# Kernel optimization log

Measured on AMD Instinct MI355X. Metric: run time of the kernel, lower is better.

## Reference

```python
import jax, jax.numpy as jnp
import numpy as np

B, S, D, H = 4, 2048, 1024, 16


def setup_inputs() -> dict:
    key = jax.random.key(0)
    ks = jax.random.split(key, 9)
    scale = 0.02  # keep logits in a sane range
    x = jax.random.normal(ks[0], (B, S, D), dtype=jnp.float32)
    Wq = jax.random.normal(ks[1], (D, D), dtype=jnp.float32) * scale
    bq = jax.random.normal(ks[2], (D,), dtype=jnp.float32) * scale
    Wk = jax.random.normal(ks[3], (D, D), dtype=jnp.float32) * scale
    bk = jax.random.normal(ks[4], (D,), dtype=jnp.float32) * scale
    Wv = jax.random.normal(ks[5], (D, D), dtype=jnp.float32) * scale
    bv = jax.random.normal(ks[6], (D,), dtype=jnp.float32) * scale
    Wo = jax.random.normal(ks[7], (D, D), dtype=jnp.float32) * scale
    bo = jax.random.normal(ks[8], (D,), dtype=jnp.float32) * scale
    return {"x": x, "Wq": Wq, "bq": bq, "Wk": Wk, "bk": bk,
            "Wv": Wv, "bv": bv, "Wo": Wo, "bo": bo}


def _apply_rope(x):
    """Rotate-half RoPE over the full feature dim (applied pre-projection)."""
    b, s, d = x.shape
    half = d // 2
    # theta_i = 10000^(-2i/d), i in [0, d/2)
    freq = jnp.exp(jnp.arange(0, d, 2, dtype=jnp.float32) * (-np.log(10000.0) / d))
    ang = jnp.arange(s, dtype=jnp.float32)[:, None] * freq[None, :]  # [S, d/2]
    cos, sin = jnp.cos(ang), jnp.sin(ang)
    x1, x2 = x[..., :half], x[..., half:]
    return jnp.concatenate([x1 * cos - x2 * sin, x1 * sin + x2 * cos], axis=-1)


def reference(x, Wq, bq, Wk, bk, Wv, bv, Wo, bo):
    b, s, d = x.shape
    h = H
    hd = d // h
    rx = _apply_rope(x)  # [B, S, D]

    def proj(W, bias):
        y = rx @ W.T + bias                       # torch Linear: x W^T + b
        return y.reshape(b, s, h, hd).transpose(0, 2, 1, 3)  # [B, H, S, hd]

    q, k, v = proj(Wq, bq), proj(Wk, bk), proj(Wv, bv)
    scores = jnp.einsum('bhqd,bhkd->bhqk', q, k) / np.sqrt(hd)
    attn = jax.nn.softmax(scores, axis=-1)
    attended = jnp.einsum('bhqk,bhkd->bhqd', attn, v)
    attended = attended.transpose(0, 2, 1, 3).reshape(b, s, d)
    return attended @ Wo.T + bo
```

## Files before the change

### kernel.cpp

```cpp
#include <hip/hip_runtime.h>

#define NB 4
#define NS 2048
#define ND 1024
#define NH 16
#define HD 64

using bf16x8 = __attribute__((ext_vector_type(8))) short;
using f32x4  = __attribute__((ext_vector_type(4))) float;

__device__ __forceinline__ unsigned short f2bf(float f) {
  union { float f; unsigned u; } a; a.f = f;
  unsigned r = a.u + 0x7FFF + ((a.u >> 16) & 1);
  return (unsigned short)(r >> 16);
}

__device__ __forceinline__ void gload_lds16(const void* g, void* l) {
  __builtin_amdgcn_global_load_lds(
      (const __attribute__((address_space(1))) void*)g,
      (__attribute__((address_space(3))) void*)l, 16, 0, 0);
}

__global__ __launch_bounds__(256) void rope_kernel(const float* __restrict__ x,
                                                   unsigned short* __restrict__ rx) {
  int idx = blockIdx.x * 256 + threadIdx.x;
  int j  = idx & 511;
  int bs = idx >> 9;
  int s  = bs & (NS - 1);
  const float* xp = x + (size_t)bs * ND;
  float ang = (float)s * __expf((float)j * -0.017988946039f);
  float sn, cs;
  __sincosf(ang, &sn, &cs);
  float x1 = xp[j], x2 = xp[j + 512];
  unsigned short* rp = rx + (size_t)bs * ND;
  rp[j]       = f2bf(x1 * cs - x2 * sn);
  rp[j + 512] = f2bf(x1 * sn + x2 * cs);
}

__global__ __launch_bounds__(256) void wconv_kernel(const float* __restrict__ w0,
                                                    const float* __restrict__ w1,
                                                    const float* __restrict__ w2,
                                                    const float* __restrict__ w3,
                                                    unsigned short* __restrict__ wb) {
  int idx = blockIdx.x * 256 + threadIdx.x;
  int e = idx << 2;
  const float* w = (e < (1 << 20)) ? w0 : (e < (2 << 20)) ? w1 : (e < (3 << 20)) ? w2 : w3;
  float4 v = *(const float4*)(w + (e & 0xFFFFF));
  ushort4 o;
  o.x = f2bf(v.x); o.y = f2bf(v.y); o.z = f2bf(v.z); o.w = f2bf(v.w);
  *(ushort4*)(wb + e) = o;
}

__global__ __launch_bounds__(256) void gemm_qkv(const unsigned short* __restrict__ A,
                                                const unsigned short* __restrict__ Wb,
                                                const float* __restrict__ bq,
                                                const float* __restrict__ bk,
                                                const float* __restrict__ bv,
                                                unsigned short* __restrict__ q,
                                                unsigned short* __restrict__ k,
                                                unsigned short* __restrict__ vt) {
  __shared__ alignas(16) unsigned short As[128 * 32];
  __shared__ alignas(16) unsigned short Bs[128 * 32];
  const int tid = threadIdx.x;
  const int lane = tid & 63;
  const int wid = tid >> 6;
  const int wm = wid >> 1, wn = wid & 1;
  const int l15 = lane & 15, lg = lane >> 4;
  const int m0 = blockIdx.x * 128;
  const int n0 = blockIdx.y * 128;
  const int z = blockIdx.z;
  const unsigned short* Bp = Wb + ((size_t)z << 20);

  f32x4 acc[4][4] = {};

  for (int k0 = 0; k0 < ND; k0 += 32) {
#pragma unroll
    for (int it = 0; it < 2; ++it) {
      int c = it * 256 + tid;
      int row = c >> 2, kc = (c & 3) << 3;
      int ldsbase = (it * 256 + (tid & 192)) << 3;
      gload_lds16(A  + (size_t)(m0 + row) * ND + k0 + kc, As + ldsbase);
      gload_lds16(Bp + (size_t)(n0 + row) * ND + k0 + kc, Bs + ldsbase);
    }
    __syncthreads();
    bf16x8 af[4], bfr[4];
#pragma unroll
    for (int m = 0; m < 4; ++m)
      af[m] = *(const bf16x8*)(As + (wm * 64 + m * 16 + l15) * 32 + lg * 8);
#pragma unroll
    for (int n = 0; n < 4; ++n)
      bfr[n] = *(const bf16x8*)(Bs + (wn * 64 + n * 16 + l15) * 32 + lg * 8);
#pragma unroll
    for (int m = 0; m < 4; ++m)
#pragma unroll
      for (int n = 0; n < 4; ++n)
        acc[m][n] = __builtin_amdgcn_mfma_f32_16x16x32_bf16(af[m], bfr[n], acc[m][n], 0, 0, 0);
    __syncthreads();
  }

  const float* bias = (z == 0) ? bq : (z == 1) ? bk : bv;
#pragma unroll
  for (int n = 0; n < 4; ++n) {
    int col = n0 + wn * 64 + n * 16 + l15;
    float bb = bias[col];
    int hh = col >> 6, dd = col & 63;
#pragma unroll
    for (int m = 0; m < 4; ++m) {
#pragma unroll
      for (int r = 0; r < 4; ++r) {
        int rowi = m0 + wm * 64 + m * 16 + lg * 4 + r;
        int bbi = rowi >> 11, ss = rowi & (NS - 1);
        unsigned short val = f2bf(acc[m][n][r] + bb);
        size_t bhoff = (size_t)(bbi * NH + hh);
        if (z == 0)      q [(bhoff * NS + ss) * HD + dd] = val;
        else if (z == 1) k [(bhoff * NS + ss) * HD + dd] = val;
        else             vt[(bhoff * HD + dd) * NS + ss] = val;
      }
    }
  }
}

__global__ __launch_bounds__(256) void attn_kernel(const unsigned short* __restrict__ q,
                                                   const unsigned short* __restrict__ k,
                                                   const unsigned short* __restrict__ vt,
                                                   unsigned short* __restrict__ att) {
  __shared__ alignas(16) unsigned short Ks[64 * 64];
  __shared__ alignas(16) unsigned short Vs[64 * 64];
  __shared__ alignas(16) unsigned short Ps[4][32 * 64];
  const int tid = threadIdx.x;
  const int lane = tid & 63;
  const int w = tid >> 6;
  const int l15 = lane & 15, lg = lane >> 4;
  const int bh = blockIdx.y;
  const int b = bh >> 4, h = bh & 15;
  const int q0 = blockIdx.x * 128;
  const unsigned short* qp = q  + (size_t)bh * NS * HD;
  const unsigned short* kp = k  + (size_t)bh * NS * HD;
  const unsigned short* vp = vt + (size_t)bh * HD * NS;

  bf16x8 qf[2][2];
#pragma unroll
  for (int m = 0; m < 2; ++m)
#pragma unroll
    for (int t = 0; t < 2; ++t)
      qf[m][t] = *(const bf16x8*)(qp + (size_t)(q0 + w * 32 + m * 16 + l15) * HD + t * 32 + lg * 8);

  f32x4 o[2][4] = {};
  float run_m[2][4], run_l[2][4];
#pragma unroll
  for (int m = 0; m < 2; ++m)
#pragma unroll
    for (int r = 0; r < 4; ++r) { run_m[m][r] = -1e30f; run_l[m][r] = 0.f; }

  unsigned short* ps = &Ps[w][0];

  for (int t0 = 0; t0 < NS; t0 += 64) {
#pragma unroll
    for (int it = 0; it < 2; ++it) {
      int c = it * 256 + tid;
      int ro = c >> 3, cc = (c & 7) << 3;
      int ldsbase = (it * 256 + (tid & 192)) << 3;
      gload_lds16(kp + (size_t)(t0 + ro) * HD + cc, Ks + ldsbase);
      gload_lds16(vp + (size_t)ro * NS + t0 + cc,   Vs + ldsbase);
    }
    __syncthreads();

    f32x4 sc[2][4] = {};
#pragma unroll
    for (int kk = 0; kk < 2; ++kk)
#pragma unroll
      for (int n = 0; n < 4; ++n) {
        bf16x8 kf = *(const bf16x8*)(Ks + (n * 16 + l15) * HD + kk * 32 + lg * 8);
#pragma unroll
        for (int m = 0; m < 2; ++m)
          sc[m][n] = __builtin_amdgcn_mfma_f32_16x16x32_bf16(qf[m][kk], kf, sc[m][n], 0, 0, 0);
      }

#pragma unroll
    for (int m = 0; m < 2; ++m)
#pragma unroll
      for (int r = 0; r < 4; ++r) {
        float mx = fmaxf(fmaxf(sc[m][0][r], sc[m][1][r]), fmaxf(sc[m][2][r], sc[m][3][r]));
        mx = fmaxf(mx, __shfl_xor(mx, 1));
        mx = fmaxf(mx, __shfl_xor(mx, 2));
        mx = fmaxf(mx, __shfl_xor(mx, 4));
        mx = fmaxf(mx, __shfl_xor(mx, 8));
        float nm = fmaxf(run_m[m][r], mx);
        float fac = __expf(0.125f * (run_m[m][r] - nm));
        run_m[m][r] = nm;
        float rs = 0.f;
#pragma unroll
        for (int n = 0; n < 4; ++n) {
          float p = __expf(0.125f * (sc[m][n][r] - nm));
          sc[m][n][r] = p;
          rs += p;
        }
        rs += __shfl_xor(rs, 1);
        rs += __shfl_xor(rs, 2);
        rs += __shfl_xor(rs, 4);
        rs += __shfl_xor(rs, 8);
        run_l[m][r] = run_l[m][r] * fac + rs;
#pragma unroll
        for (int n = 0; n < 4; ++n) o[m][n][r] *= fac;
      }

#pragma unroll
    for (int m = 0; m < 2; ++m)
#pragma unroll
      for (int n = 0; n < 4; ++n)
#pragma unroll
        for (int r = 0; r < 4; ++r)
          ps[(m * 16 + lg * 4 + r) * 64 + n * 16 + l15] = f2bf(sc[m][n][r]);

    bf16x8 pf[2][2];
#pragma unroll
    for (int m = 0; m < 2; ++m)
#pragma unroll
      for (int kk = 0; kk < 2; ++kk)
        pf[m][kk] = *(const bf16x8*)(ps + (m * 16 + l15) * 64 + kk * 32 + lg * 8);

#pragma unroll
    for (int kk = 0; kk < 2; ++kk)
#pragma unroll
      for (int n = 0; n < 4; ++n) {
        bf16x8 vf = *(const bf16x8*)(Vs + (n * 16 + l15) * HD + kk * 32 + lg * 8);
#pragma unroll
        for (int m = 0; m < 2; ++m)
          o[m][n] = __builtin_amdgcn_mfma_f32_16x16x32_bf16(pf[m][kk], vf, o[m][n], 0, 0, 0);
      }
    __syncthreads();
  }

#pragma unroll
  for (int m = 0; m < 2; ++m)
#pragma unroll
    for (int r = 0; r < 4; ++r) {
      int rowi = q0 + w * 32 + m * 16 + lg * 4 + r;
      float inv = 1.0f / run_l[m][r];
#pragma unroll
      for (int n = 0; n < 4; ++n)
        att[((size_t)(b * NS + rowi)) * ND + h * HD + n * 16 + l15] = f2bf(o[m][n][r] * inv);
    }
}

__global__ __launch_bounds__(256) void gemm_out(const unsigned short* __restrict__ A,
                                                const unsigned short* __restrict__ Bw,
                                                const float* __restrict__ bo,
                                                float* __restrict__ out) {
  __shared__ alignas(16) unsigned short As[128 * 32];
  __shared__ alignas(16) unsigned short Bs[128 * 32];
  const int tid = threadIdx.x;
  const int lane = tid & 63;
  const int wid = tid >> 6;
  const int wm = wid >> 1, wn = wid & 1;
  const int l15 = lane & 15, lg = lane >> 4;
  const int m0 = blockIdx.x * 128;
  const int n0 = blockIdx.y * 128;

  f32x4 acc[4][4] = {};

  for (int k0 = 0; k0 < ND; k0 += 32) {
#pragma unroll
    for (int it = 0; it < 2; ++it) {
      int c = it * 256 + tid;
      int row = c >> 2, kc = (c & 3) << 3;
      int ldsbase = (it * 256 + (tid & 192)) << 3;
      gload_lds16(A  + (size_t)(m0 + row) * ND + k0 + kc, As + ldsbase);
      gload_lds16(Bw + (size_t)(n0 + row) * ND + k0 + kc, Bs + ldsbase);
    }
    __syncthreads();
    bf16x8 af[4], bfr[4];
#pragma unroll
    for (int m = 0; m < 4; ++m)
      af[m] = *(const bf16x8*)(As + (wm * 64 + m * 16 + l15) * 32 + lg * 8);
#pragma unroll
    for (int n = 0; n < 4; ++n)
      bfr[n] = *(const bf16x8*)(Bs + (wn * 64 + n * 16 + l15) * 32 + lg * 8);
#pragma unroll
    for (int m = 0; m < 4; ++m)
#pragma unroll
      for (int n = 0; n < 4; ++n)
        acc[m][n] = __builtin_amdgcn_mfma_f32_16x16x32_bf16(af[m], bfr[n], acc[m][n], 0, 0, 0);
    __syncthreads();
  }

#pragma unroll
  for (int n = 0; n < 4; ++n) {
    int col = n0 + wn * 64 + n * 16 + l15;
    float bb = bo[col];
#pragma unroll
    for (int m = 0; m < 4; ++m)
#pragma unroll
      for (int r = 0; r < 4; ++r) {
        int rowi = m0 + wm * 64 + m * 16 + lg * 4 + r;
        out[(size_t)rowi * ND + col] = acc[m][n][r] + bb;
      }
  }
}

extern "C" void kernel_launch(void* const* d_in, const int* in_sizes, int n_in,
                              void* d_out, int out_size, void* d_ws, size_t ws_size,
                              hipStream_t stream) {
  const float* x  = (const float*)d_in[0];
  const float* Wq = (const float*)d_in[1];
  const float* bq = (const float*)d_in[2];
  const float* Wk = (const float*)d_in[3];
  const float* bk = (const float*)d_in[4];
  const float* Wv = (const float*)d_in[5];
  const float* bv = (const float*)d_in[6];
  const float* Wo = (const float*)d_in[7];
  const float* bo = (const float*)d_in[8];
  float* out = (float*)d_out;

  char* ws = (char*)d_ws;
  const size_t MB = 1024 * 1024;
  unsigned short* rx  = (unsigned short*)(ws);
  unsigned short* wb  = (unsigned short*)(ws + 16 * MB);
  unsigned short* qb  = (unsigned short*)(ws + 24 * MB);
  unsigned short* kb  = (unsigned short*)(ws + 40 * MB);
  unsigned short* vtb = (unsigned short*)(ws + 56 * MB);
  unsigned short* att = (unsigned short*)(ws + 72 * MB);

  rope_kernel<<<dim3(16384), dim3(256), 0, stream>>>(x, rx);
  wconv_kernel<<<dim3(4096), dim3(256), 0, stream>>>(Wq, Wk, Wv, Wo, wb);
  gemm_qkv<<<dim3(64, 8, 3), dim3(256), 0, stream>>>(rx, wb, bq, bk, bv, qb, kb, vtb);
  attn_kernel<<<dim3(16, 64), dim3(256), 0, stream>>>(qb, kb, vtb, att);
  gemm_out<<<dim3(64, 8), dim3(256), 0, stream>>>(att, wb + 3 * 1048576, bo, out);
}
```

Measured before the change: 493.9 us.

## Double-buffer K/V tiles in attention, XOR-swizzle LDS, and remap block order

The attention kernel now double-buffers the K and V tiles in shared memory and prefetches the next tile while computing on the current one. This is meant to hide global-to-LDS load latency behind the MFMA work. K, V and the P scratch buffer use an XOR swizzle on 16-byte chunks to reduce LDS bank conflicts. The grid is flattened to 1D with a swizzled mapping from block id to (batch-head, query tile), meant to improve cache locality across CUs. In exchange the kernel uses more LDS, which may lower occupancy.

```diff
diff --git a/kernel.cpp b/kernel.cpp
--- a/kernel.cpp
+++ b/kernel.cpp
@@ -124,16 +124,20 @@
                                                    const unsigned short* __restrict__ k,
                                                    const unsigned short* __restrict__ vt,
                                                    unsigned short* __restrict__ att) {
-  __shared__ alignas(16) unsigned short Ks[64 * 64];
-  __shared__ alignas(16) unsigned short Vs[64 * 64];
+  __shared__ alignas(16) unsigned short Ks[2][64 * 64];
+  __shared__ alignas(16) unsigned short Vs[2][64 * 64];
   __shared__ alignas(16) unsigned short Ps[4][32 * 64];
   const int tid = threadIdx.x;
   const int lane = tid & 63;
   const int w = tid >> 6;
   const int l15 = lane & 15, lg = lane >> 4;
-  const int bh = blockIdx.y;
+
+  const int id = blockIdx.x;
+  const int swz = (id & 7) * 128 + (id >> 3);
+  const int bh = swz >> 4;
   const int b = bh >> 4, h = bh & 15;
-  const int q0 = blockIdx.x * 128;
+  const int q0 = (swz & 15) * 128;
+
   const unsigned short* qp = q  + (size_t)bh * NS * HD;
   const unsigned short* kp = k  + (size_t)bh * NS * HD;
   const unsigned short* vp = vt + (size_t)bh * HD * NS;
@@ -154,23 +158,34 @@
 
   unsigned short* ps = &Ps[w][0];
 
+  const int c0 = tid;
+#define STAGE(buf, t0)                                                          \
+  {                                                                             \
+    _Pragma("unroll")                                                           \
+    for (int it = 0; it < 2; ++it) {                                            \
+      int c = it * 256 + c0;                                                    \
+      int ro = c >> 3;                                                          \
+      int chs = (c & 7) ^ (ro & 7);                                             \
+      int ldsbase = (it * 256 + (tid & 192)) << 3;                              \
+      gload_lds16(kp + (size_t)((t0) + ro) * HD + (chs << 3), Ks[buf] + ldsbase); \
+      gload_lds16(vp + (size_t)ro * NS + (t0) + (chs << 3),   Vs[buf] + ldsbase); \
+    }                                                                           \
+  }
+
+  STAGE(0, 0);
+  __syncthreads();
+  int cur = 0;
+
   for (int t0 = 0; t0 < NS; t0 += 64) {
-#pragma unroll
-    for (int it = 0; it < 2; ++it) {
-      int c = it * 256 + tid;
-      int ro = c >> 3, cc = (c & 7) << 3;
-      int ldsbase = (it * 256 + (tid & 192)) << 3;
-      gload_lds16(kp + (size_t)(t0 + ro) * HD + cc, Ks + ldsbase);
-      gload_lds16(vp + (size_t)ro * NS + t0 + cc,   Vs + ldsbase);
-    }
-    __syncthreads();
+    if (t0 + 64 < NS) STAGE(cur ^ 1, t0 + 64);
 
     f32x4 sc[2][4] = {};
 #pragma unroll
     for (int kk = 0; kk < 2; ++kk)
 #pragma unroll
       for (int n = 0; n < 4; ++n) {
-        bf16x8 kf = *(const bf16x8*)(Ks + (n * 16 + l15) * HD + kk * 32 + lg * 8);
+        int krow = n * 16 + l15;
+        bf16x8 kf = *(const bf16x8*)(Ks[cur] + krow * 64 + (((kk * 4 + lg) ^ (krow & 7)) << 3));
 #pragma unroll
         for (int m = 0; m < 2; ++m)
           sc[m][n] = __builtin_amdgcn_mfma_f32_16x16x32_bf16(qf[m][kk], kf, sc[m][n], 0, 0, 0);
@@ -209,27 +224,32 @@
 #pragma unroll
       for (int n = 0; n < 4; ++n)
 #pragma unroll
-        for (int r = 0; r < 4; ++r)
-          ps[(m * 16 + lg * 4 + r) * 64 + n * 16 + l15] = f2bf(sc[m][n][r]);
+        for (int r = 0; r < 4; ++r) {
+          int prow = m * 16 + lg * 4 + r;
+          ps[prow * 64 + ((n * 16 + l15) ^ ((prow & 7) << 3))] = f2bf(sc[m][n][r]);
+        }
 
     bf16x8 pf[2][2];
 #pragma unroll
     for (int m = 0; m < 2; ++m)
 #pragma unroll
       for (int kk = 0; kk < 2; ++kk)
-        pf[m][kk] = *(const bf16x8*)(ps + (m * 16 + l15) * 64 + kk * 32 + lg * 8);
+        pf[m][kk] = *(const bf16x8*)(ps + (m * 16 + l15) * 64 + (((kk * 4 + lg) ^ (l15 & 7)) << 3));
 
 #pragma unroll
     for (int kk = 0; kk < 2; ++kk)
 #pragma unroll
       for (int n = 0; n < 4; ++n) {
-        bf16x8 vf = *(const bf16x8*)(Vs + (n * 16 + l15) * HD + kk * 32 + lg * 8);
+        int vrow = n * 16 + l15;
+        bf16x8 vf = *(const bf16x8*)(Vs[cur] + vrow * 64 + (((kk * 4 + lg) ^ (vrow & 7)) << 3));
 #pragma unroll
         for (int m = 0; m < 2; ++m)
           o[m][n] = __builtin_amdgcn_mfma_f32_16x16x32_bf16(pf[m][kk], vf, o[m][n], 0, 0, 0);
       }
     __syncthreads();
-  }
+    cur ^= 1;
+  }
+#undef STAGE
 
 #pragma unroll
   for (int m = 0; m < 2; ++m)
@@ -324,6 +344,6 @@
   rope_kernel<<<dim3(16384), dim3(256), 0, stream>>>(x, rx);
   wconv_kernel<<<dim3(4096), dim3(256), 0, stream>>>(Wq, Wk, Wv, Wo, wb);
   gemm_qkv<<<dim3(64, 8, 3), dim3(256), 0, stream>>>(rx, wb, bq, bk, bv, qb, kb, vtb);
-  attn_kernel<<<dim3(16, 64), dim3(256), 0, stream>>>(qb, kb, vtb, att);
+  attn_kernel<<<dim3(1024), dim3(256), 0, stream>>>(qb, kb, vtb, att);
   gemm_out<<<dim3(64, 8), dim3(256), 0, stream>>>(att, wb + 3 * 1048576, bo, out);
 }
```

After: 427.9 us. 13.4% less time.
